# Kernel tuning notes

Hardware: AMD Instinct MI355X
Metric: run time of the kernel (lower is better)

## Reference

```python
import jax, jax.numpy as jnp
import numpy as np

D_MODEL = 1024
H = 16
D_K = D_MODEL // H
NEG = -1.0e9


def setup_inputs() -> dict:
    key = jax.random.key(0)
    ks = jax.random.split(key, 12)
    B, S = 2, 2048
    s = 1.0 / np.sqrt(D_MODEL)
    inp = {
        "q": jax.random.normal(ks[0], (B, S, D_MODEL), jnp.float32),
        "k": jax.random.normal(ks[1], (B, S, D_MODEL), jnp.float32),
        "v": jax.random.normal(ks[2], (B, S, D_MODEL), jnp.float32),
        "mask": jnp.tril(jnp.ones((S, S), jnp.int32))[None, None, :, :],
        "wq": jax.random.normal(ks[3], (D_MODEL, D_MODEL), jnp.float32) * s,
        "bq": jax.random.normal(ks[4], (D_MODEL,), jnp.float32) * s,
        "wk": jax.random.normal(ks[5], (D_MODEL, D_MODEL), jnp.float32) * s,
        "bk": jax.random.normal(ks[6], (D_MODEL,), jnp.float32) * s,
        "wv": jax.random.normal(ks[7], (D_MODEL, D_MODEL), jnp.float32) * s,
        "bv": jax.random.normal(ks[8], (D_MODEL,), jnp.float32) * s,
        "wo": jax.random.normal(ks[9], (D_MODEL, D_MODEL), jnp.float32) * s,
        "bo": jax.random.normal(ks[10], (D_MODEL,), jnp.float32) * s,
    }
    return inp


def _split_heads(x):
    # [B,S,D] -> [B,H,S,d_k]
    B, S, _ = x.shape
    return x.reshape(B, S, H, D_K).transpose(0, 2, 1, 3)


def reference(q, k, v, mask, wq, bq, wk, bk, wv, bv, wo, bo):
    # torch Linear: y = x @ W.T + b
    query = _split_heads(q @ wq.T + bq)
    key = _split_heads(k @ wk.T + bk)
    value = _split_heads(v @ wv.T + bv)
    # scores: [B,H,S,S]
    scores = jnp.einsum("bhqd,bhkd->bhqk", query, key) / jnp.sqrt(
        jnp.asarray(D_K, query.dtype))
    scores = jnp.where(mask == 0, jnp.asarray(NEG, scores.dtype), scores)
    attn = jax.nn.softmax(scores, axis=-1)  # dropout p=0.0 -> identity
    x = jnp.einsum("bhqk,bhkd->bhqd", attn, value)
    B, _, S, _ = x.shape
    x = x.transpose(0, 2, 1, 3).reshape(B, S, D_MODEL)
    return x @ wo.T + bo
```

## Files before the change

kernel.cpp:

```cpp
#include <hip/hip_runtime.h>
#include <hip/hip_bf16.h>
#include <cstdint>
#include <cstddef>

#define BATCH 2
#define SEQ   2048
#define DM    1024
#define NH    16
#define DK    64
#define MROWS (BATCH*SEQ)

typedef __bf16 bf16;
typedef float  f32x4  __attribute__((ext_vector_type(4)));
typedef bf16   bf16x8 __attribute__((ext_vector_type(8)));
typedef bf16   bf16x4 __attribute__((ext_vector_type(4)));

#define MFMA32(a, b, c) __builtin_amdgcn_mfma_f32_16x16x32_bf16(a, b, c, 0, 0, 0)

__device__ __forceinline__ void llds16(const void* gc, void* l) {
    void* g = (void*)gc;
    __builtin_amdgcn_global_load_lds(
        (__attribute__((address_space(1))) uint32_t*)g,
        (__attribute__((address_space(3))) uint32_t*)l,
        16, 0, 0);
}

__global__ __launch_bounds__(256) void k_convert(
    const float* __restrict__ q, const float* __restrict__ k, const float* __restrict__ v,
    const float* __restrict__ wq, const float* __restrict__ wk, const float* __restrict__ wv,
    const float* __restrict__ wo,
    bf16* __restrict__ qb, bf16* __restrict__ kb, bf16* __restrict__ vb,
    bf16* __restrict__ wqb, bf16* __restrict__ wkb, bf16* __restrict__ wvb,
    bf16* __restrict__ wob) {
    long t = (long)blockIdx.x * blockDim.x + threadIdx.x;
    const long NQ = (long)MROWS * DM / 4;
    const long NW = (long)DM * DM / 4;
    const float* src; bf16* dst; long off;
    if (t < NQ)            { src = q;  dst = qb;  off = t; }
    else if (t < 2*NQ)     { src = k;  dst = kb;  off = t - NQ; }
    else if (t < 3*NQ)     { src = v;  dst = vb;  off = t - 2*NQ; }
    else {
        long u = t - 3*NQ;
        if (u < NW)        { src = wq; dst = wqb; off = u; }
        else if (u < 2*NW) { src = wk; dst = wkb; off = u - NW; }
        else if (u < 3*NW) { src = wv; dst = wvb; off = u - 2*NW; }
        else               { src = wo; dst = wob; off = u - 3*NW; }
    }
    f32x4 x = *(const f32x4*)(src + off * 4);
    bf16x4 y;
    y[0] = (bf16)x[0]; y[1] = (bf16)x[1]; y[2] = (bf16)x[2]; y[3] = (bf16)x[3];
    *(bf16x4*)(dst + off * 4) = y;
}

__device__ __forceinline__ void gemm_main(const bf16* __restrict__ A, const bf16* __restrict__ B,
                                          int m0, int n0, f32x4 acc[4][4]) {
    constexpr int K = DM, BK = 32, NS = K / BK;
    __shared__ bf16 sA[2][128 * BK];
    __shared__ bf16 sB[2][128 * BK];
    const int tid = threadIdx.x;
    const int l = tid & 63, w = tid >> 6;
    const int quad = l >> 4, l15 = l & 15;
    const int wm = w & 1, wn = w >> 1;
    const int srow = l >> 2, scol = (l & 3) * 8;

#pragma unroll
    for (int i = 0; i < 2; ++i) {
        int r16 = w * 32 + i * 16;
        llds16(A + (size_t)(m0 + r16 + srow) * K + scol, &sA[0][r16 * BK]);
        llds16(B + (size_t)(n0 + r16 + srow) * K + scol, &sB[0][r16 * BK]);
    }

    for (int s = 0; s < NS; ++s) {
        __syncthreads();
        const int cur = s & 1;
        if (s + 1 < NS) {
            const int k0 = (s + 1) * BK;
#pragma unroll
            for (int i = 0; i < 2; ++i) {
                int r16 = w * 32 + i * 16;
                llds16(A + (size_t)(m0 + r16 + srow) * K + k0 + scol, &sA[cur ^ 1][r16 * BK]);
                llds16(B + (size_t)(n0 + r16 + srow) * K + k0 + scol, &sB[cur ^ 1][r16 * BK]);
            }
        }

        bf16x8 af[4], bfr[4];
#pragma unroll
        for (int mi = 0; mi < 4; ++mi)
            af[mi] = *(const bf16x8*)&sA[cur][(wm * 64 + mi * 16 + l15) * BK + quad * 8];
#pragma unroll
        for (int ni = 0; ni < 4; ++ni)
            bfr[ni] = *(const bf16x8*)&sB[cur][(wn * 64 + ni * 16 + l15) * BK + quad * 8];
#pragma unroll
        for (int mi = 0; mi < 4; ++mi)
#pragma unroll
            for (int ni = 0; ni < 4; ++ni)
                acc[mi][ni] = MFMA32(af[mi], bfr[ni], acc[mi][ni]);
    }
}

__global__ __launch_bounds__(256) void k_gemm_qkv(
    const bf16* __restrict__ qb, const bf16* __restrict__ kb, const bf16* __restrict__ vb,
    const bf16* __restrict__ wqb, const bf16* __restrict__ wkb, const bf16* __restrict__ wvb,
    const float* __restrict__ bq, const float* __restrict__ bk, const float* __restrict__ bv,
    bf16* __restrict__ Qf, bf16* __restrict__ Kf, bf16* __restrict__ Vf) {
    const int z = blockIdx.z;
    const bf16* A; const bf16* B; const float* bias;
    int m0, n0;
    if (z == 2) {
        A = vb; B = wvb; bias = bv;
        m0 = blockIdx.x * 128;
        n0 = blockIdx.y * 128;
    } else {
        A = z ? wkb : wqb; B = z ? kb : qb; bias = z ? bk : bq;
        m0 = blockIdx.y * 128;
        n0 = blockIdx.x * 128;
    }
    f32x4 acc[4][4] = {};
    gemm_main(A, B, m0, n0, acc);

    const int tid = threadIdx.x, l = tid & 63, w = tid >> 6;
    const int quad = l >> 4, l15 = l & 15;
    const int wm = w & 1, wn = w >> 1;

    if (z == 2) {
#pragma unroll
        for (int ni = 0; ni < 4; ++ni) {
            int dcol = n0 + wn * 64 + ni * 16 + l15;
            int hh2 = dcol >> 6;
            int dtile = (dcol >> 4) & 3;
            float bias_v = bias[dcol];
#pragma unroll
            for (int mi = 0; mi < 4; ++mi) {
                int srow = m0 + wm * 64 + mi * 16;
                int bb = srow >> 11, sl = srow & 2047;
                int kc = sl >> 5;
                int qp = 2 * (mi & 1) + (quad >> 1);
                bf16x4 pack;
#pragma unroll
                for (int r = 0; r < 4; ++r)
                    pack[r] = (bf16)(acc[mi][ni][r] + bias_v);
                size_t entry = ((size_t)(bb * NH + hh2) * 64 + kc) * 4 + dtile;
                *(bf16x4*)(Vf + entry * 512 + (size_t)(qp * 16 + l15) * 8 + (quad & 1) * 4) = pack;
            }
        }
    } else {
        bf16* out = z ? Kf : Qf;
        const float scale = z ? 1.0f : 0.18033688f;
        float bias_rv[4][4];
#pragma unroll
        for (int mi = 0; mi < 4; ++mi)
#pragma unroll
            for (int r = 0; r < 4; ++r)
                bias_rv[mi][r] = bias[m0 + wm * 64 + mi * 16 + quad * 4 + r];
#pragma unroll
        for (int ni = 0; ni < 4; ++ni) {
            int scol = n0 + wn * 64 + ni * 16 + l15;
            int bb = scol >> 11, s = scol & 2047;
            int s16 = s >> 4;
#pragma unroll
            for (int mi = 0; mi < 4; ++mi) {
                int drow = m0 + wm * 64 + mi * 16;
                int hh2 = (drow >> 6) & 15;
                int chunk = (drow & 63) >> 5;
                int qp = 2 * (mi & 1) + (quad >> 1);
                bf16x4 pack;
#pragma unroll
                for (int r = 0; r < 4; ++r)
                    pack[r] = (bf16)((acc[mi][ni][r] + bias_rv[mi][r]) * scale);
                size_t entry = ((size_t)(bb * NH + hh2) * 128 + s16) * 2 + chunk;
                *(bf16x4*)(out + entry * 512 + (size_t)(qp * 16 + l15) * 8 + (quad & 1) * 4) = pack;
            }
        }
    }
}

__global__ __launch_bounds__(256) void k_gemm_out(
    const bf16* __restrict__ X, const bf16* __restrict__ wob,
    const float* __restrict__ bo, float* __restrict__ out) {
    constexpr int K = DM, BK = 32, NS = K / BK;
    const int m0 = blockIdx.y * 128, n0 = blockIdx.x * 64;
    __shared__ bf16 sA[2][128 * BK];
    __shared__ bf16 sB[2][64 * BK];
    const int tid = threadIdx.x;
    const int l = tid & 63, w = tid >> 6;
    const int quad = l >> 4, l15 = l & 15;
    const int wm = w & 1, wn = w >> 1;
    const int srow = l >> 2, scol = (l & 3) * 8;

#pragma unroll
    for (int i = 0; i < 2; ++i) {
        int r16 = w * 32 + i * 16;
        llds16(X + (size_t)(m0 + r16 + srow) * K + scol, &sA[0][r16 * BK]);
    }
    llds16(wob + (size_t)(n0 + w * 16 + srow) * K + scol, &sB[0][w * 16 * BK]);

    f32x4 acc[4][2] = {};
    for (int s = 0; s < NS; ++s) {
        __syncthreads();
        const int cur = s & 1;
        if (s + 1 < NS) {
            const int k0 = (s + 1) * BK;
#pragma unroll
            for (int i = 0; i < 2; ++i) {
                int r16 = w * 32 + i * 16;
                llds16(X + (size_t)(m0 + r16 + srow) * K + k0 + scol, &sA[cur ^ 1][r16 * BK]);
            }
            llds16(wob + (size_t)(n0 + w * 16 + srow) * K + k0 + scol, &sB[cur ^ 1][w * 16 * BK]);
        }

        bf16x8 af[4], bfr[2];
#pragma unroll
        for (int mi = 0; mi < 4; ++mi)
            af[mi] = *(const bf16x8*)&sA[cur][(wm * 64 + mi * 16 + l15) * BK + quad * 8];
#pragma unroll
        for (int ni = 0; ni < 2; ++ni)
            bfr[ni] = *(const bf16x8*)&sB[cur][(wn * 32 + ni * 16 + l15) * BK + quad * 8];
#pragma unroll
        for (int mi = 0; mi < 4; ++mi)
#pragma unroll
            for (int ni = 0; ni < 2; ++ni)
                acc[mi][ni] = MFMA32(af[mi], bfr[ni], acc[mi][ni]);
    }
#pragma unroll
    for (int mi = 0; mi < 4; ++mi)
#pragma unroll
        for (int ni = 0; ni < 2; ++ni) {
            int col = n0 + wn * 32 + ni * 16 + l15;
            float bias_v = bo[col];
            int rbase = m0 + wm * 64 + mi * 16 + quad * 4;
#pragma unroll
            for (int r = 0; r < 4; ++r)
                out[(size_t)(rbase + r) * DM + col] = acc[mi][ni][r] + bias_v;
        }
}

__global__ __launch_bounds__(256, 3) void k_flash(const bf16* __restrict__ Qf,
                                                  const bf16* __restrict__ Kf,
                                                  const bf16* __restrict__ Vf,
                                                  bf16* __restrict__ X) {
    const int bh = blockIdx.x;
    const int qt = 31 - (int)blockIdx.y;
    const int b = bh >> 4, h = bh & 15;
    const int tid = threadIdx.x, w = tid >> 6, l = tid & 63;
    const int quad = l >> 4, l15 = l & 15;
    __shared__ bf16 sKV[2][16 * 512];
    __shared__ bf16 P[4][16 * 72];
    bf16* Pw = P[w];

    const bf16* qfp = Qf + (size_t)bh * 128 * 1024;
    const bf16* kfp = Kf + (size_t)bh * 128 * 1024;
    const bf16* vfp = Vf + (size_t)bh * 64 * 4 * 512;

    const int qt16 = qt * 4 + w;
    const int qglob = qt16 * 16 + l15;

    bf16x8 qf[2];
#pragma unroll
    for (int c = 0; c < 2; ++c)
        qf[c] = *(const bf16x8*)(qfp + ((size_t)qt16 * 2 + c) * 512 + (size_t)l * 8);

    f32x4 o[4] = {};
    float lp = 0.f;

#pragma unroll
    for (int i = 0; i < 4; ++i) {
        int e = w * 4 + i;
        const bf16* src = (e < 8) ? kfp + ((size_t)e) * 512
                                  : vfp + ((size_t)(e - 8)) * 512;
        llds16(src + (size_t)l * 8, &sKV[0][e * 512]);
    }

    for (int j = 0; j <= qt; ++j) {
        __syncthreads();
        const bf16* cur = sKV[j & 1];
        if (j < qt) {
            int j1 = j + 1;
#pragma unroll
            for (int i = 0; i < 4; ++i) {
                int e = w * 4 + i;
                const bf16* src = (e < 8) ? kfp + ((size_t)(j1 * 8 + e)) * 512
                                          : vfp + ((size_t)(j1 * 8 + (e - 8))) * 512;
                llds16(src + (size_t)l * 8, (void*)&sKV[j1 & 1][e * 512]);
            }
        }

        f32x4 st[4];
#pragma unroll
        for (int ni = 0; ni < 4; ++ni) {
            bf16x8 k0 = *(const bf16x8*)&cur[(size_t)(ni * 2 + 0) * 512 + l * 8];
            bf16x8 k1 = *(const bf16x8*)&cur[(size_t)(ni * 2 + 1) * 512 + l * 8];
            f32x4 zz = {};
            zz = MFMA32(k0, qf[0], zz);
            st[ni] = MFMA32(k1, qf[1], zz);
        }

        const bool diag = (j == qt);
#pragma unroll
        for (int ni = 0; ni < 4; ++ni) {
            bf16x4 ev;
#pragma unroll
            for (int r = 0; r < 4; ++r) {
                float s = st[ni][r];
                if (diag) {
                    int key = j * 64 + ni * 16 + quad * 4 + r;
                    if (key > qglob) s = -1e30f;
                }
                float e = __builtin_amdgcn_exp2f(s);
                lp += e;
                ev[r] = (bf16)e;
            }
            *(bf16x4*)&Pw[l15 * 72 + ni * 16 + quad * 4] = ev;
        }

#pragma unroll
        for (int c = 0; c < 2; ++c) {
            bf16x8 pb = *(const bf16x8*)&Pw[l15 * 72 + c * 32 + quad * 8];
#pragma unroll
            for (int dt = 0; dt < 4; ++dt) {
                bf16x8 vv = *(const bf16x8*)&cur[(size_t)(8 + c * 4 + dt) * 512 + l * 8];
                o[dt] = MFMA32(vv, pb, o[dt]);
            }
        }
    }

    lp += __shfl_xor(lp, 16, 64);
    lp += __shfl_xor(lp, 32, 64);
    float rv = 1.f / lp;

#pragma unroll
    for (int dt = 0; dt < 4; ++dt) {
        bf16x4 pk;
#pragma unroll
        for (int r = 0; r < 4; ++r)
            pk[r] = (bf16)(o[dt][r] * rv);
        *(bf16x4*)&Pw[l15 * 72 + dt * 16 + quad * 4] = pk;
    }
#pragma unroll
    for (int i = 0; i < 2; ++i) {
        int row = i * 8 + (l >> 3);
        bf16x8 vv = *(const bf16x8*)&Pw[row * 72 + (l & 7) * 8];
        *(bf16x8*)(X + (size_t)(b * SEQ + qt16 * 16 + row) * DM + h * 64 + (l & 7) * 8) = vv;
    }
}

extern "C" void kernel_launch(void* const* d_in, const int* in_sizes, int n_in,
                              void* d_out, int out_size, void* d_ws, size_t ws_size,
                              hipStream_t stream) {
    const float* q  = (const float*)d_in[0];
    const float* k  = (const float*)d_in[1];
    const float* v  = (const float*)d_in[2];
    const float* wq = (const float*)d_in[4];
    const float* bq = (const float*)d_in[5];
    const float* wk = (const float*)d_in[6];
    const float* bk = (const float*)d_in[7];
    const float* wv = (const float*)d_in[8];
    const float* bv = (const float*)d_in[9];
    const float* wo = (const float*)d_in[10];
    const float* bo = (const float*)d_in[11];
    float* out = (float*)d_out;

    uint8_t* ws = (uint8_t*)d_ws;
    const size_t SZ_ACT = (size_t)MROWS * DM * sizeof(bf16);
    const size_t SZ_W   = (size_t)DM * DM * sizeof(bf16);
    bf16* qb  = (bf16*)(ws);
    bf16* kb  = (bf16*)(ws + SZ_ACT);
    bf16* vb  = (bf16*)(ws + 2 * SZ_ACT);
    bf16* wqb = (bf16*)(ws + 3 * SZ_ACT);
    bf16* wkb = (bf16*)(ws + 3 * SZ_ACT + SZ_W);
    bf16* wvb = (bf16*)(ws + 3 * SZ_ACT + 2 * SZ_W);
    bf16* wob = (bf16*)(ws + 3 * SZ_ACT + 3 * SZ_W);
    bf16* Qf  = (bf16*)(ws + 3 * SZ_ACT + 4 * SZ_W);
    bf16* Kf  = (bf16*)(ws + 4 * SZ_ACT + 4 * SZ_W);
    bf16* Vf  = (bf16*)(ws + 5 * SZ_ACT + 4 * SZ_W);
    bf16* X   = (bf16*)(ws + 6 * SZ_ACT + 4 * SZ_W);

    {
        long total_vec4 = 3L * MROWS * DM / 4 + 4L * DM * DM / 4;
        k_convert<<<dim3((unsigned)(total_vec4 / 256)), 256, 0, stream>>>(
            q, k, v, wq, wk, wv, wo, qb, kb, vb, wqb, wkb, wvb, wob);
    }
    k_gemm_qkv<<<dim3(32, 8, 3), 256, 0, stream>>>(
        qb, kb, vb, wqb, wkb, wvb, bq, bk, bv, Qf, Kf, Vf);
    k_flash<<<dim3(BATCH * NH, SEQ / 64), 256, 0, stream>>>(Qf, Kf, Vf, X);
    k_gemm_out<<<dim3(DM / 64, MROWS / 128), 256, 0, stream>>>(X, wob, bo, out);
}
```

Measured before the change: 235.6 us.

## Fuse fp32-to-bf16 conversion into GEMM tile loads, drop convert kernel

Removes the separate conversion kernel that turned inputs and weights into bf16 copies. The QKV and output GEMMs now read fp32 directly from global memory into registers, convert to bf16, and store into the LDS double buffer after the MFMA block. This avoids writing and re-reading the bf16 intermediates and saves one launch. In exchange the GEMMs re-read fp32 tiles (twice the bytes per tile), re-convert data on every tile reuse, and give up asynchronous global-to-LDS loads in favour of register staging, which adds register pressure.

```diff
diff --git a/kernel.cpp b/kernel.cpp
--- a/kernel.cpp
+++ b/kernel.cpp
@@ -25,35 +25,15 @@
         16, 0, 0);
 }
 
-__global__ __launch_bounds__(256) void k_convert(
-    const float* __restrict__ q, const float* __restrict__ k, const float* __restrict__ v,
-    const float* __restrict__ wq, const float* __restrict__ wk, const float* __restrict__ wv,
-    const float* __restrict__ wo,
-    bf16* __restrict__ qb, bf16* __restrict__ kb, bf16* __restrict__ vb,
-    bf16* __restrict__ wqb, bf16* __restrict__ wkb, bf16* __restrict__ wvb,
-    bf16* __restrict__ wob) {
-    long t = (long)blockIdx.x * blockDim.x + threadIdx.x;
-    const long NQ = (long)MROWS * DM / 4;
-    const long NW = (long)DM * DM / 4;
-    const float* src; bf16* dst; long off;
-    if (t < NQ)            { src = q;  dst = qb;  off = t; }
-    else if (t < 2*NQ)     { src = k;  dst = kb;  off = t - NQ; }
-    else if (t < 3*NQ)     { src = v;  dst = vb;  off = t - 2*NQ; }
-    else {
-        long u = t - 3*NQ;
-        if (u < NW)        { src = wq; dst = wqb; off = u; }
-        else if (u < 2*NW) { src = wk; dst = wkb; off = u - NW; }
-        else if (u < 3*NW) { src = wv; dst = wvb; off = u - 2*NW; }
-        else               { src = wo; dst = wob; off = u - 3*NW; }
-    }
-    f32x4 x = *(const f32x4*)(src + off * 4);
-    bf16x4 y;
-    y[0] = (bf16)x[0]; y[1] = (bf16)x[1]; y[2] = (bf16)x[2]; y[3] = (bf16)x[3];
-    *(bf16x4*)(dst + off * 4) = y;
-}
-
-__device__ __forceinline__ void gemm_main(const bf16* __restrict__ A, const bf16* __restrict__ B,
-                                          int m0, int n0, f32x4 acc[4][4]) {
+__device__ __forceinline__ void cvt_store(bf16* dst, f32x4 x, f32x4 y) {
+    bf16x8 p;
+    p[0] = (bf16)x[0]; p[1] = (bf16)x[1]; p[2] = (bf16)x[2]; p[3] = (bf16)x[3];
+    p[4] = (bf16)y[0]; p[5] = (bf16)y[1]; p[6] = (bf16)y[2]; p[7] = (bf16)y[3];
+    *(bf16x8*)dst = p;
+}
+
+__device__ __forceinline__ void gemm_main_f32(const float* __restrict__ A, const float* __restrict__ B,
+                                              int m0, int n0, f32x4 acc[4][4]) {
     constexpr int K = DM, BK = 32, NS = K / BK;
     __shared__ bf16 sA[2][128 * BK];
     __shared__ bf16 sB[2][128 * BK];
@@ -61,26 +41,32 @@
     const int l = tid & 63, w = tid >> 6;
     const int quad = l >> 4, l15 = l & 15;
     const int wm = w & 1, wn = w >> 1;
-    const int srow = l >> 2, scol = (l & 3) * 8;
-
-#pragma unroll
-    for (int i = 0; i < 2; ++i) {
-        int r16 = w * 32 + i * 16;
-        llds16(A + (size_t)(m0 + r16 + srow) * K + scol, &sA[0][r16 * BK]);
-        llds16(B + (size_t)(n0 + r16 + srow) * K + scol, &sB[0][r16 * BK]);
-    }
+    const int r0 = tid >> 2, c0 = (tid & 3) * 8;
+
+    const float* pa0 = A + (size_t)(m0 + r0) * K + c0;
+    const float* pa1 = A + (size_t)(m0 + r0 + 64) * K + c0;
+    const float* pb0 = B + (size_t)(n0 + r0) * K + c0;
+    const float* pb1 = B + (size_t)(n0 + r0 + 64) * K + c0;
+
+    f32x4 La[4], Lb[4];
+    La[0] = *(const f32x4*)(pa0);     La[1] = *(const f32x4*)(pa0 + 4);
+    La[2] = *(const f32x4*)(pa1);     La[3] = *(const f32x4*)(pa1 + 4);
+    Lb[0] = *(const f32x4*)(pb0);     Lb[1] = *(const f32x4*)(pb0 + 4);
+    Lb[2] = *(const f32x4*)(pb1);     Lb[3] = *(const f32x4*)(pb1 + 4);
+    cvt_store(&sA[0][r0 * BK + c0], La[0], La[1]);
+    cvt_store(&sA[0][(r0 + 64) * BK + c0], La[2], La[3]);
+    cvt_store(&sB[0][r0 * BK + c0], Lb[0], Lb[1]);
+    cvt_store(&sB[0][(r0 + 64) * BK + c0], Lb[2], Lb[3]);
 
     for (int s = 0; s < NS; ++s) {
         __syncthreads();
         const int cur = s & 1;
+        const int k1 = (s + 1) * BK;
         if (s + 1 < NS) {
-            const int k0 = (s + 1) * BK;
-#pragma unroll
-            for (int i = 0; i < 2; ++i) {
-                int r16 = w * 32 + i * 16;
-                llds16(A + (size_t)(m0 + r16 + srow) * K + k0 + scol, &sA[cur ^ 1][r16 * BK]);
-                llds16(B + (size_t)(n0 + r16 + srow) * K + k0 + scol, &sB[cur ^ 1][r16 * BK]);
-            }
+            La[0] = *(const f32x4*)(pa0 + k1);  La[1] = *(const f32x4*)(pa0 + k1 + 4);
+            La[2] = *(const f32x4*)(pa1 + k1);  La[3] = *(const f32x4*)(pa1 + k1 + 4);
+            Lb[0] = *(const f32x4*)(pb0 + k1);  Lb[1] = *(const f32x4*)(pb0 + k1 + 4);
+            Lb[2] = *(const f32x4*)(pb1 + k1);  Lb[3] = *(const f32x4*)(pb1 + k1 + 4);
         }
 
         bf16x8 af[4], bfr[4];
@@ -95,28 +81,37 @@
 #pragma unroll
             for (int ni = 0; ni < 4; ++ni)
                 acc[mi][ni] = MFMA32(af[mi], bfr[ni], acc[mi][ni]);
+
+        if (s + 1 < NS) {
+            bf16* dA = (bf16*)&sA[cur ^ 1][0];
+            bf16* dB = (bf16*)&sB[cur ^ 1][0];
+            cvt_store(&dA[r0 * BK + c0], La[0], La[1]);
+            cvt_store(&dA[(r0 + 64) * BK + c0], La[2], La[3]);
+            cvt_store(&dB[r0 * BK + c0], Lb[0], Lb[1]);
+            cvt_store(&dB[(r0 + 64) * BK + c0], Lb[2], Lb[3]);
+        }
     }
 }
 
 __global__ __launch_bounds__(256) void k_gemm_qkv(
-    const bf16* __restrict__ qb, const bf16* __restrict__ kb, const bf16* __restrict__ vb,
-    const bf16* __restrict__ wqb, const bf16* __restrict__ wkb, const bf16* __restrict__ wvb,
+    const float* __restrict__ q, const float* __restrict__ k, const float* __restrict__ v,
+    const float* __restrict__ wq, const float* __restrict__ wk, const float* __restrict__ wv,
     const float* __restrict__ bq, const float* __restrict__ bk, const float* __restrict__ bv,
     bf16* __restrict__ Qf, bf16* __restrict__ Kf, bf16* __restrict__ Vf) {
     const int z = blockIdx.z;
-    const bf16* A; const bf16* B; const float* bias;
+    const float* A; const float* B; const float* bias;
     int m0, n0;
     if (z == 2) {
-        A = vb; B = wvb; bias = bv;
+        A = v; B = wv; bias = bv;
         m0 = blockIdx.x * 128;
         n0 = blockIdx.y * 128;
     } else {
-        A = z ? wkb : wqb; B = z ? kb : qb; bias = z ? bk : bq;
+        A = z ? wk : wq; B = z ? k : q; bias = z ? bk : bq;
         m0 = blockIdx.y * 128;
         n0 = blockIdx.x * 128;
     }
     f32x4 acc[4][4] = {};
-    gemm_main(A, B, m0, n0, acc);
+    gemm_main_f32(A, B, m0, n0, acc);
 
     const int tid = threadIdx.x, l = tid & 63, w = tid >> 6;
     const int quad = l >> 4, l15 = l & 15;
@@ -175,7 +170,7 @@
 }
 
 __global__ __launch_bounds__(256) void k_gemm_out(
-    const bf16* __restrict__ X, const bf16* __restrict__ wob,
+    const bf16* __restrict__ X, const float* __restrict__ wo,
     const float* __restrict__ bo, float* __restrict__ out) {
     constexpr int K = DM, BK = 32, NS = K / BK;
     const int m0 = blockIdx.y * 128, n0 = blockIdx.x * 64;
@@ -186,26 +181,34 @@
     const int quad = l >> 4, l15 = l & 15;
     const int wm = w & 1, wn = w >> 1;
     const int srow = l >> 2, scol = (l & 3) * 8;
+    const int rB = tid >> 2, cB = (tid & 3) * 8;
+
+    const float* pb = wo + (size_t)(n0 + rB) * K + cB;
 
 #pragma unroll
     for (int i = 0; i < 2; ++i) {
         int r16 = w * 32 + i * 16;
         llds16(X + (size_t)(m0 + r16 + srow) * K + scol, &sA[0][r16 * BK]);
     }
-    llds16(wob + (size_t)(n0 + w * 16 + srow) * K + scol, &sB[0][w * 16 * BK]);
+    {
+        f32x4 b0 = *(const f32x4*)(pb), b1 = *(const f32x4*)(pb + 4);
+        cvt_store(&sB[0][rB * BK + cB], b0, b1);
+    }
 
     f32x4 acc[4][2] = {};
+    f32x4 Lb0, Lb1;
     for (int s = 0; s < NS; ++s) {
         __syncthreads();
         const int cur = s & 1;
+        const int k1 = (s + 1) * BK;
         if (s + 1 < NS) {
-            const int k0 = (s + 1) * BK;
 #pragma unroll
             for (int i = 0; i < 2; ++i) {
                 int r16 = w * 32 + i * 16;
-                llds16(X + (size_t)(m0 + r16 + srow) * K + k0 + scol, &sA[cur ^ 1][r16 * BK]);
-            }
-            llds16(wob + (size_t)(n0 + w * 16 + srow) * K + k0 + scol, &sB[cur ^ 1][w * 16 * BK]);
+                llds16(X + (size_t)(m0 + r16 + srow) * K + k1 + scol, &sA[cur ^ 1][r16 * BK]);
+            }
+            Lb0 = *(const f32x4*)(pb + k1);
+            Lb1 = *(const f32x4*)(pb + k1 + 4);
         }
 
         bf16x8 af[4], bfr[2];
@@ -220,6 +223,9 @@
 #pragma unroll
             for (int ni = 0; ni < 2; ++ni)
                 acc[mi][ni] = MFMA32(af[mi], bfr[ni], acc[mi][ni]);
+
+        if (s + 1 < NS)
+            cvt_store(&sB[cur ^ 1][rB * BK + cB], Lb0, Lb1);
     }
 #pragma unroll
     for (int mi = 0; mi < 4; ++mi)
@@ -361,26 +367,13 @@
 
     uint8_t* ws = (uint8_t*)d_ws;
     const size_t SZ_ACT = (size_t)MROWS * DM * sizeof(bf16);
-    const size_t SZ_W   = (size_t)DM * DM * sizeof(bf16);
-    bf16* qb  = (bf16*)(ws);
-    bf16* kb  = (bf16*)(ws + SZ_ACT);
-    bf16* vb  = (bf16*)(ws + 2 * SZ_ACT);
-    bf16* wqb = (bf16*)(ws + 3 * SZ_ACT);
-    bf16* wkb = (bf16*)(ws + 3 * SZ_ACT + SZ_W);
-    bf16* wvb = (bf16*)(ws + 3 * SZ_ACT + 2 * SZ_W);
-    bf16* wob = (bf16*)(ws + 3 * SZ_ACT + 3 * SZ_W);
-    bf16* Qf  = (bf16*)(ws + 3 * SZ_ACT + 4 * SZ_W);
-    bf16* Kf  = (bf16*)(ws + 4 * SZ_ACT + 4 * SZ_W);
-    bf16* Vf  = (bf16*)(ws + 5 * SZ_ACT + 4 * SZ_W);
-    bf16* X   = (bf16*)(ws + 6 * SZ_ACT + 4 * SZ_W);
-
-    {
-        long total_vec4 = 3L * MROWS * DM / 4 + 4L * DM * DM / 4;
-        k_convert<<<dim3((unsigned)(total_vec4 / 256)), 256, 0, stream>>>(
-            q, k, v, wq, wk, wv, wo, qb, kb, vb, wqb, wkb, wvb, wob);
-    }
+    bf16* Qf = (bf16*)(ws);
+    bf16* Kf = (bf16*)(ws + SZ_ACT);
+    bf16* Vf = (bf16*)(ws + 2 * SZ_ACT);
+    bf16* X  = (bf16*)(ws + 3 * SZ_ACT);
+
     k_gemm_qkv<<<dim3(32, 8, 3), 256, 0, stream>>>(
-        qb, kb, vb, wqb, wkb, wvb, bq, bk, bv, Qf, Kf, Vf);
+        q, k, v, wq, wk, wv, bq, bk, bv, Qf, Kf, Vf);
     k_flash<<<dim3(BATCH * NH, SEQ / 64), 256, 0, stream>>>(Qf, Kf, Vf, X);
-    k_gemm_out<<<dim3(DM / 64, MROWS / 128), 256, 0, stream>>>(X, wob, bo, out);
-}
+    k_gemm_out<<<dim3(DM / 64, MROWS / 128), 256, 0, stream>>>(X, wo, bo, out);
+}
```

New measurement: 245.1 us. 1.04x slower.

## Shrink QKV GEMM tile to 128x64 and drop LDS double buffering

Applied to the files above, without the earlier changes.

The QKV projection GEMM tile goes from 128x128 to 128x64, which doubles the grid to 1536 blocks on a flattened 1D grid. The double-buffered LDS pipeline is replaced by a single buffer with two barriers per K step. The aim is more blocks for better CU occupancy and fewer registers per thread. The cost is less data reuse per block, more global traffic, and no overlap between loads and MFMA work.

```diff
diff --git a/kernel.cpp b/kernel.cpp
--- a/kernel.cpp
+++ b/kernel.cpp
@@ -52,87 +52,70 @@
     *(bf16x4*)(dst + off * 4) = y;
 }
 
-__device__ __forceinline__ void gemm_main(const bf16* __restrict__ A, const bf16* __restrict__ B,
-                                          int m0, int n0, f32x4 acc[4][4]) {
-    constexpr int K = DM, BK = 32, NS = K / BK;
-    __shared__ bf16 sA[2][128 * BK];
-    __shared__ bf16 sB[2][128 * BK];
-    const int tid = threadIdx.x;
-    const int l = tid & 63, w = tid >> 6;
-    const int quad = l >> 4, l15 = l & 15;
-    const int wm = w & 1, wn = w >> 1;
-    const int srow = l >> 2, scol = (l & 3) * 8;
-
-#pragma unroll
-    for (int i = 0; i < 2; ++i) {
-        int r16 = w * 32 + i * 16;
-        llds16(A + (size_t)(m0 + r16 + srow) * K + scol, &sA[0][r16 * BK]);
-        llds16(B + (size_t)(n0 + r16 + srow) * K + scol, &sB[0][r16 * BK]);
-    }
-
-    for (int s = 0; s < NS; ++s) {
-        __syncthreads();
-        const int cur = s & 1;
-        if (s + 1 < NS) {
-            const int k0 = (s + 1) * BK;
-#pragma unroll
-            for (int i = 0; i < 2; ++i) {
-                int r16 = w * 32 + i * 16;
-                llds16(A + (size_t)(m0 + r16 + srow) * K + k0 + scol, &sA[cur ^ 1][r16 * BK]);
-                llds16(B + (size_t)(n0 + r16 + srow) * K + k0 + scol, &sB[cur ^ 1][r16 * BK]);
-            }
-        }
-
-        bf16x8 af[4], bfr[4];
-#pragma unroll
-        for (int mi = 0; mi < 4; ++mi)
-            af[mi] = *(const bf16x8*)&sA[cur][(wm * 64 + mi * 16 + l15) * BK + quad * 8];
-#pragma unroll
-        for (int ni = 0; ni < 4; ++ni)
-            bfr[ni] = *(const bf16x8*)&sB[cur][(wn * 64 + ni * 16 + l15) * BK + quad * 8];
-#pragma unroll
-        for (int mi = 0; mi < 4; ++mi)
-#pragma unroll
-            for (int ni = 0; ni < 4; ++ni)
-                acc[mi][ni] = MFMA32(af[mi], bfr[ni], acc[mi][ni]);
-    }
-}
-
 __global__ __launch_bounds__(256) void k_gemm_qkv(
     const bf16* __restrict__ qb, const bf16* __restrict__ kb, const bf16* __restrict__ vb,
     const bf16* __restrict__ wqb, const bf16* __restrict__ wkb, const bf16* __restrict__ wvb,
     const float* __restrict__ bq, const float* __restrict__ bk, const float* __restrict__ bv,
     bf16* __restrict__ Qf, bf16* __restrict__ Kf, bf16* __restrict__ Vf) {
     const int z = blockIdx.z;
+    const int bid = blockIdx.x;
     const bf16* A; const bf16* B; const float* bias;
     int m0, n0;
     if (z == 2) {
         A = vb; B = wvb; bias = bv;
-        m0 = blockIdx.x * 128;
-        n0 = blockIdx.y * 128;
+        m0 = (bid >> 4) * 128;
+        n0 = (bid & 15) * 64;
     } else {
         A = z ? wkb : wqb; B = z ? kb : qb; bias = z ? bk : bq;
-        m0 = blockIdx.y * 128;
-        n0 = blockIdx.x * 128;
-    }
-    f32x4 acc[4][4] = {};
-    gemm_main(A, B, m0, n0, acc);
-
-    const int tid = threadIdx.x, l = tid & 63, w = tid >> 6;
+        m0 = (bid >> 6) * 128;
+        n0 = (bid & 63) * 64;
+    }
+
+    constexpr int K = DM, BK = 32;
+    __shared__ bf16 sA[128 * BK];
+    __shared__ bf16 sB[64 * BK];
+    const int tid = threadIdx.x;
+    const int l = tid & 63, w = tid >> 6;
     const int quad = l >> 4, l15 = l & 15;
     const int wm = w & 1, wn = w >> 1;
+    const int srow = l >> 2, scol = (l & 3) * 8;
+
+    f32x4 acc[4][2] = {};
+    for (int k0 = 0; k0 < K; k0 += BK) {
+#pragma unroll
+        for (int i = 0; i < 2; ++i) {
+            int r16 = w * 32 + i * 16;
+            llds16(A + (size_t)(m0 + r16 + srow) * K + k0 + scol, &sA[r16 * BK]);
+        }
+        llds16(B + (size_t)(n0 + w * 16 + srow) * K + k0 + scol, &sB[w * 16 * BK]);
+        __syncthreads();
+
+        bf16x8 af[4], bfr[2];
+#pragma unroll
+        for (int mi = 0; mi < 4; ++mi)
+            af[mi] = *(const bf16x8*)&sA[(wm * 64 + mi * 16 + l15) * BK + quad * 8];
+#pragma unroll
+        for (int ni = 0; ni < 2; ++ni)
+            bfr[ni] = *(const bf16x8*)&sB[(wn * 32 + ni * 16 + l15) * BK + quad * 8];
+#pragma unroll
+        for (int mi = 0; mi < 4; ++mi)
+#pragma unroll
+            for (int ni = 0; ni < 2; ++ni)
+                acc[mi][ni] = MFMA32(af[mi], bfr[ni], acc[mi][ni]);
+        __syncthreads();
+    }
 
     if (z == 2) {
 #pragma unroll
-        for (int ni = 0; ni < 4; ++ni) {
-            int dcol = n0 + wn * 64 + ni * 16 + l15;
+        for (int ni = 0; ni < 2; ++ni) {
+            int dcol = n0 + wn * 32 + ni * 16 + l15;
             int hh2 = dcol >> 6;
             int dtile = (dcol >> 4) & 3;
             float bias_v = bias[dcol];
 #pragma unroll
             for (int mi = 0; mi < 4; ++mi) {
-                int srow = m0 + wm * 64 + mi * 16;
-                int bb = srow >> 11, sl = srow & 2047;
+                int srw = m0 + wm * 64 + mi * 16;
+                int bb = srw >> 11, sl = srw & 2047;
                 int kc = sl >> 5;
                 int qp = 2 * (mi & 1) + (quad >> 1);
                 bf16x4 pack;
@@ -153,9 +136,9 @@
             for (int r = 0; r < 4; ++r)
                 bias_rv[mi][r] = bias[m0 + wm * 64 + mi * 16 + quad * 4 + r];
 #pragma unroll
-        for (int ni = 0; ni < 4; ++ni) {
-            int scol = n0 + wn * 64 + ni * 16 + l15;
-            int bb = scol >> 11, s = scol & 2047;
+        for (int ni = 0; ni < 2; ++ni) {
+            int scolg = n0 + wn * 32 + ni * 16 + l15;
+            int bb = scolg >> 11, s = scolg & 2047;
             int s16 = s >> 4;
 #pragma unroll
             for (int mi = 0; mi < 4; ++mi) {
@@ -379,7 +362,7 @@
         k_convert<<<dim3((unsigned)(total_vec4 / 256)), 256, 0, stream>>>(
             q, k, v, wq, wk, wv, wo, qb, kb, vb, wqb, wkb, wvb, wob);
     }
-    k_gemm_qkv<<<dim3(32, 8, 3), 256, 0, stream>>>(
+    k_gemm_qkv<<<dim3(512, 1, 3), 256, 0, stream>>>(
         qb, kb, vb, wqb, wkb, wvb, bq, bk, bv, Qf, Kf, Vf);
     k_flash<<<dim3(BATCH * NH, SEQ / 64), 256, 0, stream>>>(Qf, Kf, Vf, X);
     k_gemm_out<<<dim3(DM / 64, MROWS / 128), 256, 0, stream>>>(X, wob, bo, out);
```

New measurement: 229.7 us. 1.03x faster.
